# Performance work log

Hardware: AMD Instinct MI355X
Metric: run time of the kernel (lower is better)

The kernel has to match this reference:

```python
import jax, jax.numpy as jnp
import numpy as np

DIM_OUT = 64


def setup_inputs() -> dict:
    key = jax.random.key(0)
    k1, k2, k3, k4 = jax.random.split(key, 4)
    B, N, D_in, D_out = 4, 4096, 512, DIM_OUT
    x = jax.random.normal(k1, (B, N, D_in), dtype=jnp.float32)
    s = 1.0 / np.sqrt(D_in)
    Wk = jax.random.normal(k2, (D_out, D_in), dtype=jnp.float32) * s
    Wq = jax.random.normal(k3, (D_out, D_in), dtype=jnp.float32) * s
    Wv = jax.random.normal(k4, (D_out, D_in), dtype=jnp.float32) * s
    return {"x": x, "Wk": Wk, "Wq": Wq, "Wv": Wv}


def reference(x, Wk, Wq, Wv):
    # x: [B, N, D_in]; W*: [D_out, D_in] (torch Linear, no bias -> x @ W.T)
    keys = jnp.einsum('bnd,od->bno', x, Wk)
    queries = jnp.einsum('bnd,od->bno', x, Wq)
    values = jnp.einsum('bnd,od->bno', x, Wv)
    d_out = Wk.shape[0]
    # causal attention scores: [B, N, N]
    scores = jnp.einsum('bio,bjo->bij', queries, keys) / jnp.sqrt(jnp.float32(d_out))
    N = x.shape[1]
    causal = jnp.tril(jnp.ones((N, N), dtype=bool))  # [N, N]
    scores = jnp.where(causal[None, :, :], scores, -jnp.inf)
    att = jax.nn.softmax(scores, axis=-1)
    return jnp.einsum('bjo,bij->bio', values, att)
```

## Files before the change

### kernel.cpp

```cpp
#include <hip/hip_runtime.h>
#include <hip/hip_bf16.h>
#include <math.h>

#define N_   4096
#define DIN  512
#define D_   64

typedef __attribute__((ext_vector_type(8))) short  bf16x8;
typedef __attribute__((ext_vector_type(4))) float  f32x4;

#define ZERO4 ((f32x4){0.f, 0.f, 0.f, 0.f})

__device__ __forceinline__ unsigned short bf16rne(float x) {
    unsigned u = __float_as_uint(x);
    return (unsigned short)((u + 0x7FFFu + ((u >> 16) & 1u)) >> 16);
}
__device__ __forceinline__ unsigned cvt2(float a, float b) {
    __hip_bfloat162 h = __float22bfloat162_rn(make_float2(a, b));
    unsigned u; __builtin_memcpy(&u, &h, 4);
    return u;
}
__device__ __forceinline__ uint2 cvt4(float4 v) {
    return make_uint2(cvt2(v.x, v.y), cvt2(v.z, v.w));
}
__device__ __forceinline__ void pl32swap(unsigned &a, unsigned &b) {
    asm volatile("v_permlane32_swap_b32 %0, %1" : "+v"(a), "+v"(b));
}
__device__ __forceinline__ void pl16swap(unsigned &a, unsigned &b) {
    asm volatile("v_permlane16_swap_b32 %0, %1" : "+v"(a), "+v"(b));
}
__device__ __forceinline__ int swz(int row, int byte_in_row) {
    return (row * 128 + (byte_in_row ^ ((row & 7) << 4))) >> 1;
}

#define GLD16(gp, lp)                                                          \
    __builtin_amdgcn_global_load_lds(                                          \
        (const __attribute__((address_space(1))) unsigned int*)(gp),           \
        (__attribute__((address_space(3))) unsigned int*)(lp), 16, 0, 0)

__device__ __forceinline__ int pb128(int qi) {
    const int g = qi >> 2, r = qi & 3;
    return qi + 2 * g * (g - 1) + r * g;
}
#define PART128_F 8320

__global__ __launch_bounds__(512) void proj_kernel(
    const float* __restrict__ X, const float* __restrict__ Wk,
    const float* __restrict__ Wq, const float* __restrict__ Wv,
    unsigned short* __restrict__ Kb, unsigned short* __restrict__ Qb,
    unsigned short* __restrict__ Vt)
{
    __shared__ unsigned short Xs[2][64 * 64];
    __shared__ unsigned short Ws[2][192 * 64];

    const int tid  = threadIdx.x;
    const int lane = tid & 63;
    const int w    = tid >> 6;
    const int q15  = lane & 15;
    const int hi   = lane >> 4;
    const int rt   = w >> 1;
    const int oh   = w & 1;
    const int rbase = blockIdx.x * 64;

    float4 xr[2], wr[6];

    auto loadT = [&](int kc) {
        #pragma unroll
        for (int i = 0; i < 2; ++i) {
            const int idx = tid + i * 512;
            xr[i] = *(const float4*)(X + (size_t)(rbase + (idx >> 4)) * DIN + kc + (idx & 15) * 4);
        }
        #pragma unroll
        for (int i = 0; i < 6; ++i) {
            const int idx  = tid + i * 512;
            const int wrow = idx >> 4;
            const float* Wp = (wrow < 64)  ? Wk + (size_t)wrow * DIN
                            : (wrow < 128) ? Wq + (size_t)(wrow - 64) * DIN
                                           : Wv + (size_t)(wrow - 128) * DIN;
            wr[i] = *(const float4*)(Wp + kc + (idx & 15) * 4);
        }
    };
    auto storeT = [&](int p) {
        #pragma unroll
        for (int i = 0; i < 2; ++i) {
            const int idx = tid + i * 512;
            *(uint2*)&Xs[p][swz(idx >> 4, (idx & 15) * 8)] = cvt4(xr[i]);
        }
        #pragma unroll
        for (int i = 0; i < 6; ++i) {
            const int idx = tid + i * 512;
            *(uint2*)&Ws[p][swz(idx >> 4, (idx & 15) * 8)] = cvt4(wr[i]);
        }
    };

    f32x4 acc[6];
    #pragma unroll
    for (int i = 0; i < 6; ++i) acc[i] = ZERO4;

    loadT(0);
    int p = 0;
    for (int it = 0; it < 8; ++it) {
        storeT(p);
        __syncthreads();
        if (it < 7) loadT((it + 1) * 64);
        #pragma unroll
        for (int ks = 0; ks < 2; ++ks) {
            bf16x8 af = *(const bf16x8*)&Xs[p][swz(rt * 16 + q15, ks * 64 + hi * 16)];
            #pragma unroll
            for (int j = 0; j < 6; ++j) {
                bf16x8 bfr = *(const bf16x8*)&Ws[p][swz((oh * 6 + j) * 16 + q15, ks * 64 + hi * 16)];
                acc[j] = __builtin_amdgcn_mfma_f32_16x16x32_bf16(af, bfr, acc[j], 0, 0, 0);
            }
        }
        p ^= 1;
    }

    unsigned short* Os = &Ws[0][0];
    #pragma unroll
    for (int j = 0; j < 6; ++j) {
        const int og = oh * 6 + j;
        #pragma unroll
        for (int r = 0; r < 4; ++r) {
            const int n = rt * 16 + hi * 4 + r;
            const int o = og * 16 + q15;
            unsigned short v = bf16rne(acc[j][r]);
            if (og < 4)      Kb[(size_t)(rbase + n) * D_ + o]        = v;
            else if (og < 8) Qb[(size_t)(rbase + n) * D_ + (o - 64)] = v;
            else             Os[n * 66 + (o - 128)]                  = v;
        }
    }
    __syncthreads();
    {
        const int o  = tid >> 3;
        const int ng = (tid & 7) * 8;
        unsigned short tmp[8];
        #pragma unroll
        for (int i = 0; i < 8; ++i) tmp[i] = Os[(ng + i) * 66 + o];
        const int b  = rbase >> 12;
        const int nb = rbase & (N_ - 1);
        *(uint4*)(Vt + ((size_t)b * D_ + o) * N_ + nb + ng) = *(uint4*)&tmp[0];
    }
}

__global__ __launch_bounds__(256) void attn_part_kernel(
    const unsigned short* __restrict__ Qb, const unsigned short* __restrict__ Kb,
    const unsigned short* __restrict__ Vt, float* __restrict__ Pws)
{
    __shared__ unsigned short Ks[2][64 * 64];
    __shared__ unsigned short Vs[2][64 * 64];

    const int tid  = threadIdx.x;
    const int lane = tid & 63;
    const int w    = tid >> 6;
    const int q15  = lane & 15;
    const int hi   = lane >> 4;

    const int b = blockIdx.x & 3;
    const int u = blockIdx.x >> 2;
    const int v = 143 - u;
    int g = 0;
    #pragma unroll
    for (int t = 0; t < 7; ++t)
        if (2 * (t + 1) * (t + 2) <= v) g = t + 1;
    const int idx = v - 2 * g * (g + 1);
    const int qs  = idx / (g + 1);
    const int qi  = 4 * g + qs;
    const int sl  = idx - qs * (g + 1);

    const int nch  = 2 * qi + 2;
    const int cbeg = sl * 8;
    const int cend = min(nch, cbeg + 8);
    const int qb   = qi * 128;

    const unsigned short* Qp = Qb + (size_t)b * N_ * D_;
    const unsigned short* Kp = Kb + (size_t)b * N_ * D_;
    const unsigned short* Vp = Vt + (size_t)b * D_ * N_;

    bf16x8 qf[2][2];
    #pragma unroll
    for (int qq = 0; qq < 2; ++qq)
        #pragma unroll
        for (int ks = 0; ks < 2; ++ks)
            qf[qq][ks] = *(const bf16x8*)(Qp + (size_t)(qb + w * 32 + qq * 16 + q15) * D_ + ks * 32 + hi * 8);

    f32x4 accO[2][4];
    #pragma unroll
    for (int qq = 0; qq < 2; ++qq)
        #pragma unroll
        for (int dt = 0; dt < 4; ++dt) accO[qq][dt] = ZERO4;
    float lsum[2] = {0.f, 0.f};

    const int lsw = 8 * ((lane & 7) ^ (lane >> 3));

    auto issueChunk = [&](int p, int c) {
        const int kb2 = c * 64;
        #pragma unroll
        for (int i = 0; i < 2; ++i) {
            const int r8  = w * 2 + i;
            const int row = r8 * 8 + (lane >> 3);
            GLD16(Kp + (size_t)(kb2 + row) * D_ + lsw, &Ks[p][r8 * 512]);
            GLD16(Vp + (size_t)row * N_ + kb2 + lsw,   &Vs[p][r8 * 512]);
        }
    };

    issueChunk(0, cbeg);
    __syncthreads();

    const float SC = 0.125f * 1.44269504f;
    int p = 0;

    for (int c = cbeg; c < cend; ++c) {
        if (c + 1 < cend) issueChunk(p ^ 1, c + 1);
        const int kbase = c * 64;
        const bool edge = (c >= nch - 2);

        f32x4 sv[2][4];
        #pragma unroll
        for (int kt = 0; kt < 4; ++kt) {
            bf16x8 k0 = *(const bf16x8*)&Ks[p][swz(kt * 16 + q15, hi * 16)];
            bf16x8 k1 = *(const bf16x8*)&Ks[p][swz(kt * 16 + q15, 64 + hi * 16)];
            sv[0][kt] = __builtin_amdgcn_mfma_f32_16x16x32_bf16(k0, qf[0][0], ZERO4, 0, 0, 0);
            sv[0][kt] = __builtin_amdgcn_mfma_f32_16x16x32_bf16(k1, qf[0][1], sv[0][kt], 0, 0, 0);
            sv[1][kt] = __builtin_amdgcn_mfma_f32_16x16x32_bf16(k0, qf[1][0], ZERO4, 0, 0, 0);
            sv[1][kt] = __builtin_amdgcn_mfma_f32_16x16x32_bf16(k1, qf[1][1], sv[1][kt], 0, 0, 0);
        }

        #pragma unroll
        for (int qq = 0; qq < 2; ++qq) {
            const int qg = qb + w * 32 + qq * 16 + q15;
            unsigned pk[4][2];
            #pragma unroll
            for (int kt = 0; kt < 4; ++kt) {
                float pv[4];
                #pragma unroll
                for (int r = 0; r < 4; ++r) {
                    float vv = sv[qq][kt][r] * SC;
                    const int kg = kbase + kt * 16 + hi * 4 + r;
                    if (edge) vv = (kg <= qg) ? vv : -INFINITY;
                    pv[r] = __builtin_amdgcn_exp2f(vv);
                    lsum[qq] += pv[r];
                }
                pk[kt][0] = cvt2(pv[0], pv[1]);
                pk[kt][1] = cvt2(pv[2], pv[3]);
            }
            #pragma unroll
            for (int ks2 = 0; ks2 < 2; ++ks2) {
                unsigned a0 = pk[2 * ks2][0],     a1 = pk[2 * ks2][1];
                unsigned b0 = pk[2 * ks2 + 1][0], b1 = pk[2 * ks2 + 1][1];
                pl32swap(a0, b0);
                pl32swap(a1, b1);
                pl16swap(a0, b0);
                pl16swap(a1, b1);
                unsigned pw[4] = {a0, a1, b0, b1};
                bf16x8 pa;
                __builtin_memcpy(&pa, pw, 16);
                #pragma unroll
                for (int dt = 0; dt < 4; ++dt) {
                    bf16x8 vf = *(const bf16x8*)&Vs[p][swz(dt * 16 + q15, ks2 * 64 + hi * 16)];
                    accO[qq][dt] = __builtin_amdgcn_mfma_f32_16x16x32_bf16(pa, vf, accO[qq][dt], 0, 0, 0);
                }
            }
        }

        __syncthreads();
        p ^= 1;
    }

    #pragma unroll
    for (int qq = 0; qq < 2; ++qq) {
        lsum[qq] += __shfl_xor(lsum[qq], 16);
        lsum[qq] += __shfl_xor(lsum[qq], 32);
    }

    float* partO = Pws + ((size_t)b * 144 + pb128(qi) + sl) * PART128_F;
    #pragma unroll
    for (int qq = 0; qq < 2; ++qq) {
        #pragma unroll
        for (int dt = 0; dt < 4; ++dt)
            #pragma unroll
            for (int r = 0; r < 4; ++r)
                partO[(w * 32 + qq * 16 + hi * 4 + r) * 64 + dt * 16 + q15] = accO[qq][dt][r];
        if (hi == 0) partO[8192 + w * 32 + qq * 16 + q15] = lsum[qq];
    }
}

__global__ __launch_bounds__(256) void attn_merge_kernel(
    const float* __restrict__ Pws, float* __restrict__ O)
{
    const int tid = threadIdx.x;
    const int b   = blockIdx.x & 3;
    const int qi  = blockIdx.x >> 2;
    const int np  = (qi >> 2) + 1;
    const float* base = Pws + ((size_t)b * 144 + pb128(qi)) * PART128_F;

    const int q  = tid >> 1;
    const int dg = (tid & 1) * 32;

    float s[32];
    #pragma unroll
    for (int i = 0; i < 32; ++i) s[i] = 0.f;
    float L = 0.f;
    for (int pp = 0; pp < np; ++pp) {
        const float* sp = base + (size_t)pp * PART128_F + q * 64 + dg;
        #pragma unroll
        for (int i = 0; i < 8; ++i) {
            float4 v = *(const float4*)(sp + i * 4);
            s[4*i]   += v.x; s[4*i+1] += v.y;
            s[4*i+2] += v.z; s[4*i+3] += v.w;
        }
        L += base[(size_t)pp * PART128_F + 8192 + q];
    }
    const float rL = 1.0f / L;
    float* dst = O + ((size_t)b * N_ + qi * 128 + q) * D_ + dg;
    #pragma unroll
    for (int i = 0; i < 8; ++i)
        *(float4*)(dst + i * 4) = make_float4(s[4*i] * rL, s[4*i+1] * rL,
                                              s[4*i+2] * rL, s[4*i+3] * rL);
}

extern "C" void kernel_launch(void* const* d_in, const int* in_sizes, int n_in,
                              void* d_out, int out_size, void* d_ws, size_t ws_size,
                              hipStream_t stream)
{
    const float* x  = (const float*)d_in[0];
    const float* Wk = (const float*)d_in[1];
    const float* Wq = (const float*)d_in[2];
    const float* Wv = (const float*)d_in[3];
    float* O = (float*)d_out;

    const size_t per = (size_t)4 * N_ * D_;
    unsigned short* Kb = (unsigned short*)d_ws;
    unsigned short* Qb = Kb + per;
    unsigned short* Vt = Qb + per;
    float* Pws = (float*)((char*)d_ws + 3 * per * sizeof(unsigned short));

    proj_kernel<<<dim3(4 * N_ / 64), 512, 0, stream>>>(x, Wk, Wq, Wv, Kb, Qb, Vt);
    attn_part_kernel<<<dim3(576), 256, 0, stream>>>(Qb, Kb, Vt, Pws);
    attn_merge_kernel<<<dim3(128), 256, 0, stream>>>(Pws, O);
}
```

Baseline: 55.31 us.

## Pre-convert weights to bf16, halve projection tile, split attention into finer partials

Adds a small kernel that converts Wk/Wq/Wv to bf16 once per call. The projection kernel then reads the B fragments straight from global memory instead of staging the weights through LDS, and it now uses 32-row tiles with 256 threads, which doubles the number of blocks. The attention split shrinks each partial from 8 KV chunks to 4, giving 1088 blocks instead of 576 with a new partial-index mapping. This raises parallelism and balance, but adds an extra kernel launch, more partial-sum traffic for the merge kernel, and uncached global weight reads inside the MFMA loop.

```diff
diff --git a/kernel.cpp b/kernel.cpp
--- a/kernel.cpp
+++ b/kernel.cpp
@@ -39,19 +39,31 @@
         (__attribute__((address_space(3))) unsigned int*)(lp), 16, 0, 0)
 
 __device__ __forceinline__ int pb128(int qi) {
-    const int g = qi >> 2, r = qi & 3;
-    return qi + 2 * g * (g - 1) + r * g;
+    const int m = qi >> 1;
+    return (qi & 1) ? (m + 1) * (m + 1) : m * (m + 1);
 }
 #define PART128_F 8320
 
-__global__ __launch_bounds__(512) void proj_kernel(
-    const float* __restrict__ X, const float* __restrict__ Wk,
-    const float* __restrict__ Wq, const float* __restrict__ Wv,
+__global__ __launch_bounds__(256) void wcvt_kernel(
+    const float* __restrict__ Wk, const float* __restrict__ Wq,
+    const float* __restrict__ Wv, unsigned short* __restrict__ Wb)
+{
+    const int idx = (blockIdx.x * 256 + threadIdx.x) * 4;
+    const int row = idx >> 9;
+    const int col = idx & 511;
+    const float* src = (row < 64)  ? Wk + (size_t)row * 512 + col
+                     : (row < 128) ? Wq + (size_t)(row - 64) * 512 + col
+                                   : Wv + (size_t)(row - 128) * 512 + col;
+    float4 v = *(const float4*)src;
+    *(uint2*)&Wb[idx] = cvt4(v);
+}
+
+__global__ __launch_bounds__(256) void proj_kernel(
+    const float* __restrict__ X, const unsigned short* __restrict__ Wb,
     unsigned short* __restrict__ Kb, unsigned short* __restrict__ Qb,
     unsigned short* __restrict__ Vt)
 {
-    __shared__ unsigned short Xs[2][64 * 64];
-    __shared__ unsigned short Ws[2][192 * 64];
+    __shared__ unsigned short Xs[2][32 * 64];
 
     const int tid  = threadIdx.x;
     const int lane = tid & 63;
@@ -60,62 +72,50 @@
     const int hi   = lane >> 4;
     const int rt   = w >> 1;
     const int oh   = w & 1;
-    const int rbase = blockIdx.x * 64;
-
-    float4 xr[2], wr[6];
-
-    auto loadT = [&](int kc) {
+    const int rbase = blockIdx.x * 32;
+
+    float4 xr[2];
+    auto loadX = [&](int kc) {
         #pragma unroll
         for (int i = 0; i < 2; ++i) {
-            const int idx = tid + i * 512;
+            const int idx = tid + i * 256;
             xr[i] = *(const float4*)(X + (size_t)(rbase + (idx >> 4)) * DIN + kc + (idx & 15) * 4);
         }
-        #pragma unroll
-        for (int i = 0; i < 6; ++i) {
-            const int idx  = tid + i * 512;
-            const int wrow = idx >> 4;
-            const float* Wp = (wrow < 64)  ? Wk + (size_t)wrow * DIN
-                            : (wrow < 128) ? Wq + (size_t)(wrow - 64) * DIN
-                                           : Wv + (size_t)(wrow - 128) * DIN;
-            wr[i] = *(const float4*)(Wp + kc + (idx & 15) * 4);
-        }
     };
-    auto storeT = [&](int p) {
+    auto storeX = [&](int p) {
         #pragma unroll
         for (int i = 0; i < 2; ++i) {
-            const int idx = tid + i * 512;
+            const int idx = tid + i * 256;
             *(uint2*)&Xs[p][swz(idx >> 4, (idx & 15) * 8)] = cvt4(xr[i]);
         }
-        #pragma unroll
-        for (int i = 0; i < 6; ++i) {
-            const int idx = tid + i * 512;
-            *(uint2*)&Ws[p][swz(idx >> 4, (idx & 15) * 8)] = cvt4(wr[i]);
-        }
     };
 
     f32x4 acc[6];
     #pragma unroll
     for (int i = 0; i < 6; ++i) acc[i] = ZERO4;
 
-    loadT(0);
+    loadX(0);
     int p = 0;
     for (int it = 0; it < 8; ++it) {
-        storeT(p);
+        storeX(p);
         __syncthreads();
-        if (it < 7) loadT((it + 1) * 64);
+        if (it < 7) loadX((it + 1) * 64);
+        const int kc = it * 64;
         #pragma unroll
         for (int ks = 0; ks < 2; ++ks) {
             bf16x8 af = *(const bf16x8*)&Xs[p][swz(rt * 16 + q15, ks * 64 + hi * 16)];
             #pragma unroll
             for (int j = 0; j < 6; ++j) {
-                bf16x8 bfr = *(const bf16x8*)&Ws[p][swz((oh * 6 + j) * 16 + q15, ks * 64 + hi * 16)];
+                bf16x8 bfr = *(const bf16x8*)(Wb + (size_t)((oh * 6 + j) * 16 + q15) * DIN
+                                              + kc + ks * 32 + hi * 8);
                 acc[j] = __builtin_amdgcn_mfma_f32_16x16x32_bf16(af, bfr, acc[j], 0, 0, 0);
             }
         }
+        __syncthreads();
         p ^= 1;
     }
 
-    unsigned short* Os = &Ws[0][0];
+    unsigned short* Os = &Xs[0][0];
     #pragma unroll
     for (int j = 0; j < 6; ++j) {
         const int og = oh * 6 + j;
@@ -131,8 +131,8 @@
     }
     __syncthreads();
     {
-        const int o  = tid >> 3;
-        const int ng = (tid & 7) * 8;
+        const int o  = tid >> 2;
+        const int ng = (tid & 3) * 8;
         unsigned short tmp[8];
         #pragma unroll
         for (int i = 0; i < 8; ++i) tmp[i] = Os[(ng + i) * 66 + o];
@@ -157,19 +157,15 @@
 
     const int b = blockIdx.x & 3;
     const int u = blockIdx.x >> 2;
-    const int v = 143 - u;
-    int g = 0;
-    #pragma unroll
-    for (int t = 0; t < 7; ++t)
-        if (2 * (t + 1) * (t + 2) <= v) g = t + 1;
-    const int idx = v - 2 * g * (g + 1);
-    const int qs  = idx / (g + 1);
-    const int qi  = 4 * g + qs;
-    const int sl  = idx - qs * (g + 1);
+    const int v = 271 - u;
+    int qi = 0;
+    for (int t = 1; t < 32; ++t)
+        if (pb128(t) <= v) qi = t;
+    const int sl = v - pb128(qi);
 
     const int nch  = 2 * qi + 2;
-    const int cbeg = sl * 8;
-    const int cend = min(nch, cbeg + 8);
+    const int cbeg = sl * 4;
+    const int cend = min(nch, cbeg + 4);
     const int qb   = qi * 128;
 
     const unsigned short* Qp = Qb + (size_t)b * N_ * D_;
@@ -272,7 +268,7 @@
         lsum[qq] += __shfl_xor(lsum[qq], 32);
     }
 
-    float* partO = Pws + ((size_t)b * 144 + pb128(qi) + sl) * PART128_F;
+    float* partO = Pws + ((size_t)b * 272 + pb128(qi) + sl) * PART128_F;
     #pragma unroll
     for (int qq = 0; qq < 2; ++qq) {
         #pragma unroll
@@ -290,8 +286,8 @@
     const int tid = threadIdx.x;
     const int b   = blockIdx.x & 3;
     const int qi  = blockIdx.x >> 2;
-    const int np  = (qi >> 2) + 1;
-    const float* base = Pws + ((size_t)b * 144 + pb128(qi)) * PART128_F;
+    const int np  = (qi + 2) >> 1;
+    const float* base = Pws + ((size_t)b * 272 + pb128(qi)) * PART128_F;
 
     const int q  = tid >> 1;
     const int dg = (tid & 1) * 32;
@@ -332,9 +328,11 @@
     unsigned short* Kb = (unsigned short*)d_ws;
     unsigned short* Qb = Kb + per;
     unsigned short* Vt = Qb + per;
-    float* Pws = (float*)((char*)d_ws + 3 * per * sizeof(unsigned short));
-
-    proj_kernel<<<dim3(4 * N_ / 64), 512, 0, stream>>>(x, Wk, Wq, Wv, Kb, Qb, Vt);
-    attn_part_kernel<<<dim3(576), 256, 0, stream>>>(Qb, Kb, Vt, Pws);
+    unsigned short* Wb = Vt + per;
+    float* Pws = (float*)((char*)d_ws + (3 * per + 192 * 512) * sizeof(unsigned short));
+
+    wcvt_kernel<<<dim3(96), 256, 0, stream>>>(Wk, Wq, Wv, Wb);
+    proj_kernel<<<dim3(4 * N_ / 32), 256, 0, stream>>>(x, Wb, Kb, Qb, Vt);
+    attn_part_kernel<<<dim3(1088), 256, 0, stream>>>(Qb, Kb, Vt, Pws);
     attn_merge_kernel<<<dim3(128), 256, 0, stream>>>(Pws, O);
 }
```

New measurement: 77.11 us. 1.39x slower.
